# Optimization experiments

Hardware: AMD Instinct MI355X
Metric: run time of the kernel (lower is better)

## Reference

```python
import jax, jax.numpy as jnp
import numpy as np

MAX_TOTAL = 20        # max_total_size
MAX_PER_CLASS = 20    # max_output_size_per_class
SCORE_TH = 0.5        # score_threshold
IOU_TH = 0.5          # tf combined NMS default iou_threshold
K_CAND = 200          # top candidates per class considered for NMS
VARIANCES = jnp.array([0.1, 0.1, 0.2, 0.2], jnp.float32)


def setup_inputs() -> dict:
    key = jax.random.key(0)
    k1, k2, k3, k4, k5, k6 = jax.random.split(key, 6)
    B, N, C = 64, 8732, 21
    pred_deltas = jax.random.normal(k1, (B, N, 4), jnp.float32)
    pred_labels = jax.random.uniform(k2, (B, N, C), dtype=jnp.float32)
    # synthetic normalized anchors (y1,x1,y2,x2) with valid extents
    cy = jax.random.uniform(k3, (N,), dtype=jnp.float32)
    cx = jax.random.uniform(k4, (N,), dtype=jnp.float32)
    h = jax.random.uniform(k5, (N,), dtype=jnp.float32, minval=0.05, maxval=0.3)
    w = jax.random.uniform(k6, (N,), dtype=jnp.float32, minval=0.05, maxval=0.3)
    anchors = jnp.stack([cy - h / 2, cx - w / 2, cy + h / 2, cx + w / 2], axis=-1)
    return {"pred_deltas": pred_deltas, "pred_labels": pred_labels, "anchors": anchors}


def _decode(anchors, deltas):
    # anchors [N,4] (y1,x1,y2,x2); deltas [B,N,4] (dy,dx,dh,dw) -> boxes [B,N,4]
    ah = anchors[:, 2] - anchors[:, 0]
    aw = anchors[:, 3] - anchors[:, 1]
    acy = anchors[:, 0] + 0.5 * ah
    acx = anchors[:, 1] + 0.5 * aw
    cy = deltas[..., 0] * ah + acy
    cx = deltas[..., 1] * aw + acx
    h = jnp.exp(deltas[..., 2]) * ah
    w = jnp.exp(deltas[..., 3]) * aw
    return jnp.stack([cy - 0.5 * h, cx - 0.5 * w, cy + 0.5 * h, cx + 0.5 * w], axis=-1)


def _pairwise_iou(boxes):
    # boxes [K,4] -> iou [K,K]
    y1, x1, y2, x2 = boxes[:, 0], boxes[:, 1], boxes[:, 2], boxes[:, 3]
    area = (y2 - y1) * (x2 - x1)
    ih = jnp.clip(jnp.minimum(y2[:, None], y2[None, :]) - jnp.maximum(y1[:, None], y1[None, :]), 0.0)
    iw = jnp.clip(jnp.minimum(x2[:, None], x2[None, :]) - jnp.maximum(x1[:, None], x1[None, :]), 0.0)
    inter = ih * iw
    return inter / (area[:, None] + area[None, :] - inter + 1e-8)


def _nms_one_class(scores, boxes):
    # scores [N], boxes [N,4] -> (top scores [MAX_PER_CLASS], boxes [MAX_PER_CLASS,4])
    vals, idx = jax.lax.top_k(scores, K_CAND)          # sorted desc
    cboxes = boxes[idx]                                # [K,4]
    iou = _pairwise_iou(cboxes)                        # [K,K]
    valid = vals > SCORE_TH
    ar = jnp.arange(K_CAND)

    def body(i, keep):
        suppressed = jnp.any(keep & (iou[i] > IOU_TH) & (ar < i))
        return keep.at[i].set(valid[i] & ~suppressed)

    keep = jax.lax.fori_loop(0, K_CAND, body, jnp.zeros(K_CAND, dtype=bool))
    kept_scores = jnp.where(keep, vals, 0.0)
    top_vals, top_i = jax.lax.top_k(kept_scores, MAX_PER_CLASS)
    return top_vals, cboxes[top_i]


def reference(pred_deltas, pred_labels, anchors):
    deltas = pred_deltas * VARIANCES                       # variance scaling
    boxes = _decode(anchors, deltas)                       # [B,N,4]
    # zero out all class scores where argmax class == 0 (background)
    lab_map = jnp.argmax(pred_labels, axis=-1, keepdims=True)
    scores = jnp.where(lab_map != 0, pred_labels, 0.0)     # [B,N,C]

    per_class = jax.vmap(_nms_one_class, in_axes=(1, None))   # over classes
    per_batch = jax.vmap(per_class, in_axes=(0, 0))           # over batch
    cls_scores, cls_boxes = per_batch(scores, boxes)          # [B,C,P], [B,C,P,4]

    B, C, P = cls_scores.shape
    flat_scores = cls_scores.reshape(B, C * P)
    flat_boxes = cls_boxes.reshape(B, C * P, 4)
    class_ids = jnp.broadcast_to(jnp.arange(C, dtype=jnp.float32)[:, None], (C, P)).reshape(-1)

    top_vals, top_i = jax.lax.top_k(flat_scores, MAX_TOTAL)   # [B,MAX_TOTAL]
    final_boxes = jnp.take_along_axis(flat_boxes, top_i[..., None], axis=1)
    final_boxes = jnp.clip(final_boxes, 0.0, 1.0)             # combined NMS clip_boxes=True
    valid = top_vals > 0.0
    final_boxes = jnp.where(valid[..., None], final_boxes, 0.0)
    final_labels = jnp.where(valid, class_ids[top_i], 0.0)
    return final_boxes, top_vals, final_labels
```

## Files before the change

kernel.cpp:

```cpp
#include <hip/hip_runtime.h>
#include <stdint.h>

typedef unsigned long long u64;
typedef unsigned int u32;
typedef unsigned short u16;

#define BATCH 64
#define NANCH 8732
#define NPAD  8736
#define NCHUNK 1092
#define NCLS 21
#define KCAND 200
#define PPC 20
#define PTOT 20

__global__ __launch_bounds__(256) void kdecode(
    const float* __restrict__ labels,
    unsigned char* __restrict__ msk, u16* __restrict__ st16, int useT)
{
#pragma clang fp contract(off)
    int n = blockIdx.x * 256 + threadIdx.x;
    int b = blockIdx.y;
    if (n >= NPAD) return;
    if (n >= NANCH) {
        if (useT) {
#pragma unroll
            for (int c = 0; c < NCLS; ++c)
                st16[((size_t)b * NCLS + c) * NPAD + n] = 0;
        }
        return;
    }
    const float* lab = labels + ((size_t)b * NANCH + n) * NCLS;
    float v[NCLS];
#pragma unroll
    for (int c = 0; c < NCLS; ++c) v[c] = lab[c];
    float mx = v[0]; int am = 0;
#pragma unroll
    for (int c = 1; c < NCLS; ++c) if (v[c] > mx) { mx = v[c]; am = c; }
    bool mk = (am != 0);
    msk[(size_t)b * NANCH + n] = mk ? 1 : 0;
    if (useT) {
#pragma unroll
        for (int c = 0; c < NCLS; ++c) {
            u16 t = mk ? (u16)(u32)(v[c] * 65536.0f) : (u16)0;
            st16[((size_t)b * NCLS + c) * NPAD + n] = t;
        }
    }
}

__device__ __forceinline__ u64 shflxor64(u64 x, int m) {
    return (u64)__shfl_xor((long long)x, m, 64);
}

__device__ __forceinline__ void suffixFind(const u32* hist, u32* waveTot, int nb, int need,
                                           int* sSel, int* sAbove, int* sH, int* sTot,
                                           int tid, int lane, int wv)
{
    int K = (nb + 255) >> 8;
    int base = tid * K;
    u32 own = 0;
    for (int q = 0; q < K; ++q) { int bi = base + q; own += (bi < nb) ? hist[bi] : 0u; }
    u32 s = own;
#pragma unroll
    for (int d = 1; d < 64; d <<= 1) {
        u32 o = __shfl_down(s, d, 64);
        if (lane + d < 64) s += o;
    }
    if (lane == 0) waveTot[wv] = s;
    __syncthreads();
    if (tid == 0 && sTot) *sTot = (int)(waveTot[0] + waveTot[1] + waveTot[2] + waveTot[3]);
    u32 add = 0;
    for (int w = wv + 1; w < 4; ++w) add += waveTot[w];
    u32 cum = (s - own) + add;
    for (int q = K - 1; q >= 0; --q) {
        int bi = base + q;
        u32 hh = (bi < nb) ? hist[bi] : 0u;
        if (cum < (u32)need && cum + hh >= (u32)need) { *sSel = bi; *sAbove = (int)cum; *sH = (int)hh; }
        cum += hh;
    }
    __syncthreads();
}

__global__ __launch_bounds__(256) void knms(
    const float* __restrict__ labels, const unsigned char* __restrict__ msk,
    const u16* __restrict__ st16,
    const float* __restrict__ deltas, const float* __restrict__ anchors,
    float* __restrict__ clsScores, float* __restrict__ clsBoxes, int useT)
{
#pragma clang fp contract(off)
    __shared__ __align__(16) char smem[8192];
    u32*   hist = (u32*)smem;
    float* cbY1 = (float*)smem;
    float* cbX1 = (float*)(smem + 1024);
    float* cbY2 = (float*)(smem + 2048);
    float* cbX2 = (float*)(smem + 3072);
    float* cbAr = (float*)(smem + 4096);
    float* cVal = (float*)(smem + 5120);
    u64*   iouT = (u64*)(smem + 6144);
    __shared__ u64 candKey[256];
    __shared__ u32 waveTot[4];
    __shared__ float outS[PPC];
    __shared__ float outB[PPC * 4];
    __shared__ int sSel, sAbove, sH, sTot, sN, sKP;

    const int tid = threadIdx.x;
    const int lane = tid & 63;
    const int wv = tid >> 6;
    const int bc = blockIdx.x;
    const int b = bc / NCLS;
    const int c = bc % NCLS;

    uint4 rc[5];
    if (useT) {
        const uint4* src = (const uint4*)(st16 + (size_t)bc * NPAD);
#pragma unroll
        for (int q = 0; q < 5; ++q) {
            int i4 = q * 256 + tid;
            rc[q] = (i4 < NCHUNK) ? src[i4] : make_uint4(0, 0, 0, 0);
        }
    } else {
        for (int q = 0; q < 5; ++q) {
            int chunk = q * 256 + tid;
            u32 w4[4] = {0, 0, 0, 0};
            if (chunk < NCHUNK) {
                for (int w = 0; w < 4; ++w)
                    for (int h = 0; h < 2; ++h) {
                        int n = chunk * 8 + w * 2 + h;
                        u32 t = 0;
                        if (n < NANCH && msk[(size_t)b * NANCH + n]) {
                            float v = labels[((size_t)b * NANCH + n) * NCLS + c];
                            t = (u32)(v * 65536.0f);
                        }
                        w4[w] |= t << (16 * h);
                    }
            }
            rc[q] = make_uint4(w4[0], w4[1], w4[2], w4[3]);
        }
    }

    for (int q = tid; q < 1024; q += 256) hist[1024 + q] = 0;
    if (tid == 0) { sSel = -1; sAbove = 0; sH = 0; sTot = 0; sN = 0; sKP = 0; }
    __syncthreads();
#pragma unroll
    for (int q = 0; q < 5; ++q) {
        if (q * 256 + tid < NCHUNK) {
            u32 w4[4] = {rc[q].x, rc[q].y, rc[q].z, rc[q].w};
#pragma unroll
            for (int w = 0; w < 4; ++w) {
                u32 lo = w4[w] & 0xFFFFu, hi = w4[w] >> 16;
                if (lo & 0x8000u) atomicAdd(&hist[lo >> 5], 1u);
                if (hi & 0x8000u) atomicAdd(&hist[hi >> 5], 1u);
            }
        }
    }
    __syncthreads();
    suffixFind(hist + 1024, waveTot, 1024, KCAND, &sSel, &sAbove, &sH, &sTot, tid, lane, wv);

    int A, cnt; u32 T16;
    if (sTot < KCAND) { T16 = 32768u; A = 0; cnt = sTot; }
    else { A = sAbove; T16 = (u32)(1024 + sSel) << 5; cnt = A + sH; }

    if (cnt > 256) {
        if (tid < 32) hist[tid] = 0;
        if (tid == 0) { sSel = -1; sAbove = 0; sH = 0; }
        __syncthreads();
#pragma unroll
        for (int q = 0; q < 5; ++q) {
            if (q * 256 + tid < NCHUNK) {
                u32 w4[4] = {rc[q].x, rc[q].y, rc[q].z, rc[q].w};
#pragma unroll
                for (int w = 0; w < 4; ++w) {
                    u32 lo = w4[w] & 0xFFFFu, hi = w4[w] >> 16;
                    if (lo >= T16 && lo < T16 + 32) atomicAdd(&hist[lo - T16], 1u);
                    if (hi >= T16 && hi < T16 + 32) atomicAdd(&hist[hi - T16], 1u);
                }
            }
        }
        __syncthreads();
        suffixFind(hist, waveTot, 32, KCAND - A, &sSel, &sAbove, &sH, nullptr, tid, lane, wv);
        A += sAbove;
        T16 += (u32)sSel;
        cnt = A + sH;
    }

#pragma unroll
    for (int q = 0; q < 5; ++q) {
        int chunk = q * 256 + tid;
        if (chunk < NCHUNK) {
            u32 w4[4] = {rc[q].x, rc[q].y, rc[q].z, rc[q].w};
#pragma unroll
            for (int w = 0; w < 4; ++w) {
#pragma unroll
                for (int h = 0; h < 2; ++h) {
                    u32 t = (h == 0) ? (w4[w] & 0xFFFFu) : (w4[w] >> 16);
                    if (t >= T16) {
                        int n = chunk * 8 + w * 2 + h;
                        float v = labels[((size_t)b * NANCH + n) * NCLS + c];
                        int slot = atomicAdd(&sN, 1);
                        if (slot < 256)
                            candKey[slot] = ((u64)__float_as_uint(v) << 32) | (u32)(~(u32)n);
                    }
                }
            }
        }
    }
    __syncthreads();
    int nc = sN; if (nc > 256) nc = 256;

    u64 x = (tid < nc) ? candKey[tid] : 0ull;
    for (int k = 2; k <= 256; k <<= 1) {
        for (int j = k >> 1; j > 0; j >>= 1) {
            u64 y;
            if (j < 64) {
                y = shflxor64(x, j);
            } else {
                __syncthreads();
                candKey[tid] = x;
                __syncthreads();
                y = candKey[tid ^ j];
            }
            bool keepMax = ((tid & k) == 0) == ((tid & j) == 0);
            u64 mx = (x > y) ? x : y;
            u64 mn = (x > y) ? y : x;
            x = keepMax ? mx : mn;
        }
    }

    float myV = __uint_as_float((u32)(x >> 32));
    float myY1 = 0.f, myX1 = 0.f, myY2 = 0.f, myX2 = 0.f, myAr = 0.f;
    u32 idx = ~(u32)x;
    if (tid < KCAND && idx < (u32)NANCH) {
        float4 d = ((const float4*)deltas)[(size_t)b * NANCH + idx];
        float4 a = ((const float4*)anchors)[idx];
        float ah = a.z - a.x, aw = a.w - a.y;
        float acy = a.x + 0.5f * ah, acx = a.y + 0.5f * aw;
        float cy = (d.x * 0.1f) * ah + acy;
        float cx = (d.y * 0.1f) * aw + acx;
        float hh2 = expf(d.z * 0.2f) * ah;
        float ww2 = expf(d.w * 0.2f) * aw;
        myY1 = cy - 0.5f * hh2; myX1 = cx - 0.5f * ww2;
        myY2 = cy + 0.5f * hh2; myX2 = cx + 0.5f * ww2;
        myAr = (myY2 - myY1) * (myX2 - myX1);
    } else {
        myV = 0.f;
    }
    __syncthreads();
    cbY1[tid] = myY1; cbX1[tid] = myX1; cbY2[tid] = myY2; cbX2[tid] = myX2;
    cbAr[tid] = myAr; cVal[tid] = myV;

    u64 k0 = 0, k1 = 0, k2 = 0, k3 = 0;
    int KPw = 0;
    for (int t0 = 0; t0 < 4; ++t0) {
        __syncthreads();
        if (sKP >= PPC) break;
        int rowBase = t0 * 64;
        int rows = KCAND - rowBase; if (rows > 64) rows = 64;
        for (int r = wv; r < rows; r += 4) {
            int i = rowBase + r;
            float y1i = cbY1[i], x1i = cbX1[i], y2i = cbY2[i], x2i = cbX2[i], ari = cbAr[i];
            for (int cg = 0; cg <= t0; ++cg) {
                int j = cg * 64 + lane;
                float ih = fminf(y2i, cbY2[j]) - fmaxf(y1i, cbY1[j]);
                ih = fmaxf(ih, 0.0f);
                float iw = fminf(x2i, cbX2[j]) - fmaxf(x1i, cbX1[j]);
                iw = fmaxf(iw, 0.0f);
                float inter = ih * iw;
                float iou = inter / (ari + cbAr[j] - inter + 1e-8f);
                u64 bal = __ballot(iou > 0.5f);
                if (lane == 0) iouT[r * 4 + cg] = bal;
            }
        }
        __syncthreads();
        if (tid < 64) {
            int i = rowBase + lane;
            u64 r0 = 0, r1 = 0, r2 = 0, r3 = 0;
            bool vld = false;
            if (lane < rows) {
                r0 = iouT[lane * 4 + 0]; r1 = iouT[lane * 4 + 1];
                r2 = iouT[lane * 4 + 2]; r3 = iouT[lane * 4 + 3];
                vld = cVal[i] > 0.5f;
            }
            for (int l = 0; l < rows; ++l) {
                int mydec = (vld && !((k0 & r0) | (k1 & r1) | (k2 & r2) | (k3 & r3))) ? 1 : 0;
                int d = __shfl(mydec, l, 64);
                if (d) {
                    u64 bit = 1ull << l;
                    if (t0 == 0) k0 |= bit; else if (t0 == 1) k1 |= bit;
                    else if (t0 == 2) k2 |= bit; else k3 |= bit;
                    ++KPw;
                    if (KPw >= PPC) break;
                }
            }
            if (tid == 0) sKP = KPw;
        }
    }
    __syncthreads();

    if (tid < PPC) outS[tid] = 0.0f;
    if (tid < PPC * 4) outB[tid] = 0.0f;
    __syncthreads();

    if (tid < 64) {
        int base = 0;
#pragma unroll
        for (int chunk = 0; chunk < 4; ++chunk) {
            u64 kw = (chunk == 0) ? k0 : (chunk == 1) ? k1 : (chunk == 2) ? k2 : k3;
            int i = chunk * 64 + tid;
            bool kept = ((kw >> tid) & 1ull) != 0;
            int rank = base + (int)__popcll(kw & ((1ull << tid) - 1ull));
            if (kept && rank < PPC && i < KCAND) {
                outS[rank] = cVal[i];
                outB[rank * 4 + 0] = cbY1[i];
                outB[rank * 4 + 1] = cbX1[i];
                outB[rank * 4 + 2] = cbY2[i];
                outB[rank * 4 + 3] = cbX2[i];
            }
            base += (int)__popcll(kw);
        }
    }
    __syncthreads();
    if (tid < PPC) clsScores[(size_t)bc * PPC + tid] = outS[tid];
    if (tid < PPC * 4) clsBoxes[(size_t)bc * PPC * 4 + tid] = outB[tid];
}

__global__ __launch_bounds__(512) void kmerge(
    const float* __restrict__ clsScores, const float* __restrict__ clsBoxes,
    float* __restrict__ out)
{
#pragma clang fp contract(off)
    __shared__ u64 key[512];
    const int tid = threadIdx.x;
    const int b = blockIdx.x;
    const int F = NCLS * PPC;
    u64 kk = 0;
    if (tid < F) {
        float v = clsScores[(size_t)b * F + tid];
        kk = ((u64)__float_as_uint(v) << 32) | (u32)(~(u32)tid);
    }
    key[tid] = kk;
    for (int k = 2; k <= 512; k <<= 1)
        for (int j = k >> 1; j > 0; j >>= 1) {
            __syncthreads();
            int ixj = tid ^ j;
            if (ixj > tid) {
                u64 a = key[tid], bb = key[ixj];
                if (((tid & k) == 0) ? (a < bb) : (a > bb)) { key[tid] = bb; key[ixj] = a; }
            }
        }
    __syncthreads();
    if (tid < PTOT) {
        u64 kx = key[tid];
        float v = __uint_as_float((u32)(kx >> 32));
        u32 f = ~((u32)kx);
        bool valid = (v > 0.0f) && (f < (u32)F);
        float cls = valid ? (float)(f / PPC) : 0.0f;
        float* oB = out;
        float* oV = out + (size_t)BATCH * PTOT * 4;
        float* oL = oV + (size_t)BATCH * PTOT;
#pragma unroll
        for (int q = 0; q < 4; ++q) {
            float xq = 0.0f;
            if (valid) {
                xq = clsBoxes[((size_t)b * F + f) * 4 + q];
                xq = fminf(fmaxf(xq, 0.0f), 1.0f);
            }
            oB[((size_t)b * PTOT + tid) * 4 + q] = xq;
        }
        oV[(size_t)b * PTOT + tid] = v;
        oL[(size_t)b * PTOT + tid] = cls;
    }
}

extern "C" void kernel_launch(void* const* d_in, const int* in_sizes, int n_in,
                              void* d_out, int out_size, void* d_ws, size_t ws_size,
                              hipStream_t stream)
{
    const float* deltas  = (const float*)d_in[0];
    const float* labels  = (const float*)d_in[1];
    const float* anchors = (const float*)d_in[2];
    float* out = (float*)d_out;
    char* ws = (char*)d_ws;

    const size_t mskOff = 0;
    const size_t csOff  = 558848;
    const size_t cbOff  = 666368;
    const size_t stOff  = 1096448;
    const size_t needT  = 24578816;

    unsigned char* msk = (unsigned char*)(ws + mskOff);
    float* clsScores = (float*)(ws + csOff);
    float* clsBoxes  = (float*)(ws + cbOff);
    u16* st16        = (u16*)(ws + stOff);
    int useT = (ws_size >= needT) ? 1 : 0;

    dim3 gA((NPAD + 255) / 256, BATCH);
    kdecode<<<gA, 256, 0, stream>>>(labels, msk, st16, useT);
    knms<<<BATCH * NCLS, 256, 0, stream>>>(labels, msk, st16, deltas, anchors,
                                           clsScores, clsBoxes, useT);
    kmerge<<<BATCH, 512, 0, stream>>>(clsScores, clsBoxes, out);
}
```

Baseline: 57.95 us.

## Compact high-score candidates into per-class lists instead of dense score matrix

```diff
diff --git a/kernel.cpp b/kernel.cpp
--- a/kernel.cpp
+++ b/kernel.cpp
@@ -7,43 +7,71 @@
 
 #define BATCH 64
 #define NANCH 8732
-#define NPAD  8736
 #define NCHUNK 1092
 #define NCLS 21
 #define KCAND 200
+#define CAP 2048
 #define PPC 20
 #define PTOT 20
+#define PRETHR 0.9f
+
+__global__ __launch_bounds__(256) void kzero(u32* __restrict__ cnt)
+{
+    int i = blockIdx.x * 256 + threadIdx.x;
+    if (i < BATCH * NCLS) cnt[i] = 0;
+}
 
 __global__ __launch_bounds__(256) void kdecode(
     const float* __restrict__ labels,
-    unsigned char* __restrict__ msk, u16* __restrict__ st16, int useT)
+    unsigned char* __restrict__ msk, u64* __restrict__ lists,
+    u32* __restrict__ cnt, int useT)
 {
 #pragma clang fp contract(off)
-    int n = blockIdx.x * 256 + threadIdx.x;
-    int b = blockIdx.y;
-    if (n >= NPAD) return;
-    if (n >= NANCH) {
-        if (useT) {
-#pragma unroll
-            for (int c = 0; c < NCLS; ++c)
-                st16[((size_t)b * NCLS + c) * NPAD + n] = 0;
-        }
-        return;
-    }
-    const float* lab = labels + ((size_t)b * NANCH + n) * NCLS;
+    const int n = blockIdx.x * 256 + threadIdx.x;
+    const int b = blockIdx.y;
+    const int lane = threadIdx.x & 63;
+    const bool active = (n < NANCH);
+
     float v[NCLS];
 #pragma unroll
-    for (int c = 0; c < NCLS; ++c) v[c] = lab[c];
-    float mx = v[0]; int am = 0;
-#pragma unroll
-    for (int c = 1; c < NCLS; ++c) if (v[c] > mx) { mx = v[c]; am = c; }
-    bool mk = (am != 0);
-    msk[(size_t)b * NANCH + n] = mk ? 1 : 0;
-    if (useT) {
-#pragma unroll
-        for (int c = 0; c < NCLS; ++c) {
-            u16 t = mk ? (u16)(u32)(v[c] * 65536.0f) : (u16)0;
-            st16[((size_t)b * NCLS + c) * NPAD + n] = t;
+    for (int c = 0; c < NCLS; ++c) v[c] = 0.0f;
+    bool mk = false;
+    if (active) {
+        const float* lab = labels + ((size_t)b * NANCH + n) * NCLS;
+#pragma unroll
+        for (int c = 0; c < NCLS; ++c) v[c] = lab[c];
+        float mx = v[0]; int am = 0;
+#pragma unroll
+        for (int c = 1; c < NCLS; ++c) if (v[c] > mx) { mx = v[c]; am = c; }
+        mk = (am != 0);
+        msk[(size_t)b * NANCH + n] = mk ? 1 : 0;
+    }
+    if (!useT) return;
+
+    u32 myHits = 0;
+#pragma unroll
+    for (int c = 0; c < NCLS; ++c)
+        if (active && mk && v[c] >= PRETHR) myHits |= (1u << c);
+
+    u32 myCnt = 0;
+#pragma unroll
+    for (int c = 0; c < NCLS; ++c) {
+        u64 m = __ballot((myHits >> c) & 1u);
+        if (lane == c) myCnt = (u32)__popcll(m);
+    }
+    u32 myBase = 0;
+    if (lane < NCLS) myBase = atomicAdd(&cnt[b * NCLS + lane], myCnt);
+
+#pragma unroll
+    for (int c = 0; c < NCLS; ++c) {
+        u64 m = __ballot((myHits >> c) & 1u);
+        u32 base = (u32)__shfl((int)myBase, c, 64);
+        if ((m >> lane) & 1ull) {
+            u32 rank = (u32)__popcll(m & ((1ull << lane) - 1ull));
+            u32 slot = base + rank;
+            if (slot < CAP)
+                lists[((size_t)b * NCLS + c) * CAP + slot] =
+                    ((u64)__float_as_uint(v[c]) << 32) | (u32)(~(u32)n);
         }
     }
 }
@@ -83,7 +111,7 @@
 
 __global__ __launch_bounds__(256) void knms(
     const float* __restrict__ labels, const unsigned char* __restrict__ msk,
-    const u16* __restrict__ st16,
+    const u64* __restrict__ lists, const u32* __restrict__ cnt,
     const float* __restrict__ deltas, const float* __restrict__ anchors,
     float* __restrict__ clsScores, float* __restrict__ clsBoxes, int useT)
 {
@@ -110,15 +138,64 @@
     const int b = bc / NCLS;
     const int c = bc % NCLS;
 
-    uint4 rc[5];
-    if (useT) {
-        const uint4* src = (const uint4*)(st16 + (size_t)bc * NPAD);
-#pragma unroll
-        for (int q = 0; q < 5; ++q) {
-            int i4 = q * 256 + tid;
-            rc[q] = (i4 < NCHUNK) ? src[i4] : make_uint4(0, 0, 0, 0);
+    const int nTHR = useT ? (int)cnt[bc] : -1;
+    const bool fast = useT && (nTHR >= KCAND) && (nTHR <= CAP);
+
+    if (fast) {
+        const u64* lst = lists + (size_t)bc * CAP;
+        u64 kr[8];
+#pragma unroll
+        for (int q = 0; q < 8; ++q) {
+            int i = q * 256 + tid;
+            kr[q] = (i < nTHR) ? lst[i] : 0ull;
+        }
+        for (int q = tid; q < 1024; q += 256) hist[1024 + q] = 0;
+        if (tid == 0) { sSel = -1; sAbove = 0; sH = 0; sN = 0; sKP = 0; }
+        __syncthreads();
+#pragma unroll
+        for (int q = 0; q < 8; ++q) {
+            if (q * 256 + tid < nTHR) {
+                float v = __uint_as_float((u32)(kr[q] >> 32));
+                u32 t = (u32)(v * 65536.0f);
+                atomicAdd(&hist[t >> 5], 1u);
+            }
+        }
+        __syncthreads();
+        suffixFind(hist + 1024, waveTot, 1024, KCAND, &sSel, &sAbove, &sH, nullptr, tid, lane, wv);
+        int A = sAbove;
+        u32 T16 = (u32)(1024 + sSel) << 5;
+        int cnt2 = A + sH;
+
+        if (cnt2 > 256) {
+            if (tid < 32) hist[tid] = 0;
+            if (tid == 0) { sSel = -1; sAbove = 0; sH = 0; }
+            __syncthreads();
+#pragma unroll
+            for (int q = 0; q < 8; ++q) {
+                if (q * 256 + tid < nTHR) {
+                    float v = __uint_as_float((u32)(kr[q] >> 32));
+                    u32 t = (u32)(v * 65536.0f);
+                    if (t >= T16 && t < T16 + 32) atomicAdd(&hist[t - T16], 1u);
+                }
+            }
+            __syncthreads();
+            suffixFind(hist, waveTot, 32, KCAND - A, &sSel, &sAbove, &sH, nullptr, tid, lane, wv);
+            A += sAbove;
+            T16 += (u32)sSel;
+        }
+#pragma unroll
+        for (int q = 0; q < 8; ++q) {
+            if (q * 256 + tid < nTHR) {
+                float v = __uint_as_float((u32)(kr[q] >> 32));
+                u32 t = (u32)(v * 65536.0f);
+                if (t >= T16) {
+                    int slot = atomicAdd(&sN, 1);
+                    if (slot < 256) candKey[slot] = kr[q];
+                }
+            }
         }
     } else {
+        uint4 rc[5];
         for (int q = 0; q < 5; ++q) {
             int chunk = q * 256 + tid;
             u32 w4[4] = {0, 0, 0, 0};
@@ -136,33 +213,8 @@
             }
             rc[q] = make_uint4(w4[0], w4[1], w4[2], w4[3]);
         }
-    }
-
-    for (int q = tid; q < 1024; q += 256) hist[1024 + q] = 0;
-    if (tid == 0) { sSel = -1; sAbove = 0; sH = 0; sTot = 0; sN = 0; sKP = 0; }
-    __syncthreads();
-#pragma unroll
-    for (int q = 0; q < 5; ++q) {
-        if (q * 256 + tid < NCHUNK) {
-            u32 w4[4] = {rc[q].x, rc[q].y, rc[q].z, rc[q].w};
-#pragma unroll
-            for (int w = 0; w < 4; ++w) {
-                u32 lo = w4[w] & 0xFFFFu, hi = w4[w] >> 16;
-                if (lo & 0x8000u) atomicAdd(&hist[lo >> 5], 1u);
-                if (hi & 0x8000u) atomicAdd(&hist[hi >> 5], 1u);
-            }
-        }
-    }
-    __syncthreads();
-    suffixFind(hist + 1024, waveTot, 1024, KCAND, &sSel, &sAbove, &sH, &sTot, tid, lane, wv);
-
-    int A, cnt; u32 T16;
-    if (sTot < KCAND) { T16 = 32768u; A = 0; cnt = sTot; }
-    else { A = sAbove; T16 = (u32)(1024 + sSel) << 5; cnt = A + sH; }
-
-    if (cnt > 256) {
-        if (tid < 32) hist[tid] = 0;
-        if (tid == 0) { sSel = -1; sAbove = 0; sH = 0; }
+        for (int q = tid; q < 1024; q += 256) hist[1024 + q] = 0;
+        if (tid == 0) { sSel = -1; sAbove = 0; sH = 0; sTot = 0; sN = 0; sKP = 0; }
         __syncthreads();
 #pragma unroll
         for (int q = 0; q < 5; ++q) {
@@ -171,34 +223,54 @@
 #pragma unroll
                 for (int w = 0; w < 4; ++w) {
                     u32 lo = w4[w] & 0xFFFFu, hi = w4[w] >> 16;
-                    if (lo >= T16 && lo < T16 + 32) atomicAdd(&hist[lo - T16], 1u);
-                    if (hi >= T16 && hi < T16 + 32) atomicAdd(&hist[hi - T16], 1u);
-                }
-            }
-        }
-        __syncthreads();
-        suffixFind(hist, waveTot, 32, KCAND - A, &sSel, &sAbove, &sH, nullptr, tid, lane, wv);
-        A += sAbove;
-        T16 += (u32)sSel;
-        cnt = A + sH;
-    }
-
-#pragma unroll
-    for (int q = 0; q < 5; ++q) {
-        int chunk = q * 256 + tid;
-        if (chunk < NCHUNK) {
-            u32 w4[4] = {rc[q].x, rc[q].y, rc[q].z, rc[q].w};
-#pragma unroll
-            for (int w = 0; w < 4; ++w) {
-#pragma unroll
-                for (int h = 0; h < 2; ++h) {
-                    u32 t = (h == 0) ? (w4[w] & 0xFFFFu) : (w4[w] >> 16);
-                    if (t >= T16) {
-                        int n = chunk * 8 + w * 2 + h;
-                        float v = labels[((size_t)b * NANCH + n) * NCLS + c];
-                        int slot = atomicAdd(&sN, 1);
-                        if (slot < 256)
-                            candKey[slot] = ((u64)__float_as_uint(v) << 32) | (u32)(~(u32)n);
+                    if (lo & 0x8000u) atomicAdd(&hist[lo >> 5], 1u);
+                    if (hi & 0x8000u) atomicAdd(&hist[hi >> 5], 1u);
+                }
+            }
+        }
+        __syncthreads();
+        suffixFind(hist + 1024, waveTot, 1024, KCAND, &sSel, &sAbove, &sH, &sTot, tid, lane, wv);
+        int A; int cnt2; u32 T16;
+        if (sTot < KCAND) { T16 = 32768u; A = 0; cnt2 = sTot; }
+        else { A = sAbove; T16 = (u32)(1024 + sSel) << 5; cnt2 = A + sH; }
+        if (cnt2 > 256) {
+            if (tid < 32) hist[tid] = 0;
+            if (tid == 0) { sSel = -1; sAbove = 0; sH = 0; }
+            __syncthreads();
+#pragma unroll
+            for (int q = 0; q < 5; ++q) {
+                if (q * 256 + tid < NCHUNK) {
+                    u32 w4[4] = {rc[q].x, rc[q].y, rc[q].z, rc[q].w};
+#pragma unroll
+                    for (int w = 0; w < 4; ++w) {
+                        u32 lo = w4[w] & 0xFFFFu, hi = w4[w] >> 16;
+                        if (lo >= T16 && lo < T16 + 32) atomicAdd(&hist[lo - T16], 1u);
+                        if (hi >= T16 && hi < T16 + 32) atomicAdd(&hist[hi - T16], 1u);
+                    }
+                }
+            }
+            __syncthreads();
+            suffixFind(hist, waveTot, 32, KCAND - A, &sSel, &sAbove, &sH, nullptr, tid, lane, wv);
+            A += sAbove;
+            T16 += (u32)sSel;
+        }
+#pragma unroll
+        for (int q = 0; q < 5; ++q) {
+            int chunk = q * 256 + tid;
+            if (chunk < NCHUNK) {
+                u32 w4[4] = {rc[q].x, rc[q].y, rc[q].z, rc[q].w};
+#pragma unroll
+                for (int w = 0; w < 4; ++w) {
+#pragma unroll
+                    for (int h = 0; h < 2; ++h) {
+                        u32 t = (h == 0) ? (w4[w] & 0xFFFFu) : (w4[w] >> 16);
+                        if (t >= T16) {
+                            int n = chunk * 8 + w * 2 + h;
+                            float v = labels[((size_t)b * NANCH + n) * NCLS + c];
+                            int slot = atomicAdd(&sN, 1);
+                            if (slot < 256)
+                                candKey[slot] = ((u64)__float_as_uint(v) << 32) | (u32)(~(u32)n);
+                        }
                     }
                 }
             }
@@ -381,21 +453,24 @@
     float* out = (float*)d_out;
     char* ws = (char*)d_ws;
 
-    const size_t mskOff = 0;
-    const size_t csOff  = 558848;
-    const size_t cbOff  = 666368;
-    const size_t stOff  = 1096448;
-    const size_t needT  = 24578816;
+    const size_t mskOff  = 0;
+    const size_t cntOff  = 558848;
+    const size_t csOff   = 564480;
+    const size_t cbOff   = 672000;
+    const size_t listOff = 1102336;
+    const size_t needT   = 23122432;
 
     unsigned char* msk = (unsigned char*)(ws + mskOff);
+    u32* cnt         = (u32*)(ws + cntOff);
     float* clsScores = (float*)(ws + csOff);
     float* clsBoxes  = (float*)(ws + cbOff);
-    u16* st16        = (u16*)(ws + stOff);
+    u64* lists       = (u64*)(ws + listOff);
     int useT = (ws_size >= needT) ? 1 : 0;
 
-    dim3 gA((NPAD + 255) / 256, BATCH);
-    kdecode<<<gA, 256, 0, stream>>>(labels, msk, st16, useT);
-    knms<<<BATCH * NCLS, 256, 0, stream>>>(labels, msk, st16, deltas, anchors,
+    if (useT) kzero<<<(BATCH * NCLS + 255) / 256, 256, 0, stream>>>(cnt);
+    dim3 gA((NANCH + 255) / 256, BATCH);
+    kdecode<<<gA, 256, 0, stream>>>(labels, msk, lists, cnt, useT);
+    knms<<<BATCH * NCLS, 256, 0, stream>>>(labels, msk, lists, cnt, deltas, anchors,
                                            clsScores, clsBoxes, useT);
     kmerge<<<BATCH, 512, 0, stream>>>(clsScores, clsBoxes, out);
 }
```

Measured after the change: 58.55 us. No clear change (+1.0%).
